# Optimization experiments

Measured on AMD Instinct MI355X. Metric: run time of the kernel, lower is better.

Reference implementation:

```python
import jax, jax.numpy as jnp
import numpy as np


def setup_inputs() -> dict:
    key = jax.random.key(0)
    k1, k2, k3 = jax.random.split(key, 3)
    d = 256
    x = jax.random.normal(k1, (8, 2048, d), dtype=jnp.float32)
    # torch nn.Linear(d, d, bias=False) weights, shape [out, in]
    Wq = jax.random.normal(k2, (d, d), dtype=jnp.float32) * (d ** -0.5)
    Wk = jax.random.normal(k3, (d, d), dtype=jnp.float32) * (d ** -0.5)
    return {"x": x, "Wq": Wq, "Wk": Wk}


def reference(x, Wq, Wk):
    # q = x @ Wq^T, k = x @ Wk^T (torch Linear convention), v = x (raw context)
    d = x.shape[-1]
    scale = d ** -0.5
    q = jnp.einsum('bnd,ed->bne', x, Wq)
    k = jnp.einsum('bnd,ed->bne', x, Wk)
    sim = jnp.einsum('bid,bjd->bij', q, k) * scale  # [b, n, n]
    attn = jax.nn.softmax(sim, axis=-1)
    out = jnp.einsum('bij,bjd->bid', attn, x)
    return out
```

## Files before the change

### kernel.cpp

```cpp
#include <hip/hip_runtime.h>
#include <hip/hip_bf16.h>

#define BB 8
#define NN 2048
#define DD 256

typedef _Float16 half8 __attribute__((ext_vector_type(8)));
typedef _Float16 half4 __attribute__((ext_vector_type(4)));
typedef float f32x4 __attribute__((ext_vector_type(4)));
typedef unsigned int uint4v __attribute__((ext_vector_type(4)));

#define GLDS(gsrc, ldst) __builtin_amdgcn_global_load_lds( \
    (const __attribute__((address_space(1))) void*)(gsrc), \
    (__attribute__((address_space(3))) void*)(ldst), 16, 0, 0)

__device__ __forceinline__ half8 cvt8(const float* __restrict__ p) {
    f32x4 a = *(const f32x4*)p;
    f32x4 b = *(const f32x4*)(p + 4);
    half8 h;
    h[0] = (_Float16)a[0]; h[1] = (_Float16)a[1];
    h[2] = (_Float16)a[2]; h[3] = (_Float16)a[3];
    h[4] = (_Float16)b[0]; h[5] = (_Float16)b[1];
    h[6] = (_Float16)b[2]; h[7] = (_Float16)b[3];
    return h;
}

__global__ void __launch_bounds__(256)
qk_proj(const float* __restrict__ x, const float* __restrict__ Wq,
        const float* __restrict__ Wk, _Float16* __restrict__ qh,
        _Float16* __restrict__ kh, _Float16* __restrict__ xT) {
    __shared__ __align__(16) _Float16 Wql[16][264];
    __shared__ __align__(16) _Float16 Wkl[16][264];
    const int tid = threadIdx.x;
    const int wave = tid >> 6, lane = tid & 63;
    const int g = lane >> 4, l16 = lane & 15;
    const int rowblk = blockIdx.x >> 1, thalf = blockIdx.x & 1;
    const size_t r0 = ((size_t)rowblk * 4 + wave) * 16;

    half8 xa[8];
#pragma unroll
    for (int c = 0; c < 8; ++c)
        xa[c] = cvt8(x + (r0 + l16) * DD + c * 32 + g * 8);

    {
        const int gt = (int)(r0 + l16);
        const int bb = gt >> 11, nn = gt & 2047;
        _Float16* xtb = xT + (size_t)bb * DD * NN + nn;
        if (thalf == 0) {
#pragma unroll
            for (int c = 0; c < 4; ++c)
#pragma unroll
                for (int j = 0; j < 8; ++j)
                    xtb[(size_t)(c * 32 + g * 8 + j) * NN] = xa[c][j];
        } else {
#pragma unroll
            for (int c = 4; c < 8; ++c)
#pragma unroll
                for (int j = 0; j < 8; ++j)
                    xtb[(size_t)(c * 32 + g * 8 + j) * NN] = xa[c][j];
        }
    }

    for (int i = 0; i < 8; ++i) {
        const int t = thalf * 8 + i;
        __syncthreads();
        {
            const int sel = tid >> 7;
            const int tt  = tid & 127;
            const int row = tt >> 3;
            const int col = (tt & 7) * 32;
            const float* src = (sel ? Wk : Wq) + (size_t)(t * 16 + row) * DD + col;
            _Float16* dst = sel ? &Wkl[row][col] : &Wql[row][col];
#pragma unroll
            for (int j = 0; j < 4; ++j)
                *(half8*)(dst + j * 8) = cvt8(src + j * 8);
        }
        __syncthreads();
        f32x4 aq = {0.f, 0.f, 0.f, 0.f}, ak = {0.f, 0.f, 0.f, 0.f};
#pragma unroll
        for (int c = 0; c < 8; ++c) {
            half8 bq = *(const half8*)&Wql[l16][c * 32 + g * 8];
            half8 bk = *(const half8*)&Wkl[l16][c * 32 + g * 8];
            aq = __builtin_amdgcn_mfma_f32_16x16x32_f16(xa[c], bq, aq, 0, 0, 0);
            ak = __builtin_amdgcn_mfma_f32_16x16x32_f16(xa[c], bk, ak, 0, 0, 0);
        }
#pragma unroll
        for (int r = 0; r < 4; ++r) {
            size_t row = r0 + g * 4 + r;
            qh[row * DD + t * 16 + l16] = (_Float16)(aq[r] * 0.0625f);
            kh[row * DD + t * 16 + l16] = (_Float16)ak[r];
        }
    }
}

__global__ void __launch_bounds__(512)
attn(const _Float16* __restrict__ qh, const _Float16* __restrict__ kh,
     const _Float16* __restrict__ xT, float* __restrict__ out,
     _Float16* __restrict__ Op, float* __restrict__ ml, int lgS) {
    __shared__ __align__(16) _Float16 Kl[2][32 * 256];
    __shared__ __align__(16) _Float16 Vl[3][256 * 32];
    const int tid = threadIdx.x;
    const int wave = tid >> 6, lane = tid & 63;
    const int g = lane >> 4, l16 = lane & 15;
    const int S = 1 << lgS;
    const int b = blockIdx.x & 7;
    const int tt = blockIdx.x >> 3;
    const int s = tt & (S - 1);
    const int qb = tt >> lgS;
    const int wq0 = qb * 256 + wave * 32;
    const int kvlen = NN >> lgS;
    const int kv_begin = s * kvlen;
    const int nt = kvlen >> 5;

    const _Float16* qp = qh + ((size_t)b * NN + wq0) * DD;
    const _Float16* kb = kh + (size_t)b * NN * DD;
    const _Float16* vb = xT + (size_t)b * DD * NN;

    int krow[2], koff[2], vrow[2];
#pragma unroll
    for (int j = 0; j < 2; ++j) {
        int rp = 8 * j + wave;
        int T = 2 * rp + (lane >> 5);
        krow[j] = 8 * ((T >> 2) & 3) + 4 * (T >> 4) + (T & 3);
        koff[j] = ((lane & 31) * 8) ^ ((T & 7) << 3);
        vrow[j] = 16 * rp + (lane >> 2);
    }
    const int voff = (lane & 3) * 8;

    half8 qf[2][8];
#pragma unroll
    for (int t = 0; t < 2; ++t)
#pragma unroll
        for (int c = 0; c < 8; ++c)
            qf[t][c] = *(const half8*)(qp + (size_t)(t * 16 + l16) * DD + c * 32 + g * 8);

    f32x4 O[2][16];
    f32x4 zero = {0.f, 0.f, 0.f, 0.f};
#pragma unroll
    for (int t = 0; t < 2; ++t)
#pragma unroll
        for (int dt = 0; dt < 16; ++dt) O[t][dt] = zero;
    float m[2] = {-1e30f, -1e30f};
    float l[2] = {0.f, 0.f};
    half8 paA[2], paB[2];

    f32x4 s00, s01, s10, s11;
    auto qkt = [&](int tau) {
        const _Float16* Klb = Kl[tau & 1];
        s00 = zero; s01 = zero; s10 = zero; s11 = zero;
        const int swz = (l16 & 7) << 3;
#pragma unroll
        for (int c = 0; c < 8; ++c) {
            int u = (c * 32 + g * 8) ^ swz;
            half8 k0 = *(const half8*)&Klb[l16 * 256 + u];
            half8 k1 = *(const half8*)&Klb[(16 + l16) * 256 + u];
            s00 = __builtin_amdgcn_mfma_f32_16x16x32_f16(k0, qf[0][c], s00, 0, 0, 0);
            s01 = __builtin_amdgcn_mfma_f32_16x16x32_f16(k1, qf[0][c], s01, 0, 0, 0);
            s10 = __builtin_amdgcn_mfma_f32_16x16x32_f16(k0, qf[1][c], s10, 0, 0, 0);
            s11 = __builtin_amdgcn_mfma_f32_16x16x32_f16(k1, qf[1][c], s11, 0, 0, 0);
        }
    };

    auto pv = [&](int tau, half8 (&paIn)[2]) {
        const _Float16* Vlb = Vl[tau % 3];
#pragma unroll
        for (int dt = 0; dt < 16; ++dt) {
            half8 vf = *(const half8*)&Vlb[(dt * 16 + l16) * 32 + g * 8];
            O[0][dt] = __builtin_amdgcn_mfma_f32_16x16x32_f16(paIn[0], vf, O[0][dt], 0, 0, 0);
            O[1][dt] = __builtin_amdgcn_mfma_f32_16x16x32_f16(paIn[1], vf, O[1][dt], 0, 0, 0);
        }
    };

    auto smax = [&](half8 (&paOut)[2]) {
        float tm[2];
#pragma unroll
        for (int t = 0; t < 2; ++t) {
            const f32x4& a = t ? s10 : s00;
            const f32x4& c = t ? s11 : s01;
            float v = fmaxf(fmaxf(fmaxf(a[0], a[1]), fmaxf(a[2], a[3])),
                            fmaxf(fmaxf(c[0], c[1]), fmaxf(c[2], c[3])));
            v = fmaxf(v, __shfl_xor(v, 16));
            v = fmaxf(v, __shfl_xor(v, 32));
            tm[t] = v;
        }
        bool need = (tm[0] > m[0] + 8.f) || (tm[1] > m[1] + 8.f);
        if (__ballot(need)) {
#pragma unroll
            for (int t = 0; t < 2; ++t) {
                float nm = fmaxf(m[t], tm[t]);
                float al = __expf(m[t] - nm);
                m[t] = nm;
                l[t] *= al;
                float alr[4];
#pragma unroll
                for (int r = 0; r < 4; ++r) alr[r] = __shfl(al, g * 4 + r);
#pragma unroll
                for (int dt = 0; dt < 16; ++dt)
#pragma unroll
                    for (int r = 0; r < 4; ++r) O[t][dt][r] *= alr[r];
            }
        }
#pragma unroll
        for (int t = 0; t < 2; ++t) {
            f32x4 e0, e1;
            const f32x4& a = t ? s10 : s00;
            const f32x4& c = t ? s11 : s01;
#pragma unroll
            for (int r = 0; r < 4; ++r) {
                e0[r] = __expf(a[r] - m[t]);
                e1[r] = __expf(c[r] - m[t]);
            }
            float rs = (e0[0] + e0[1]) + (e0[2] + e0[3]) +
                       (e1[0] + e1[1]) + (e1[2] + e1[3]);
            rs += __shfl_xor(rs, 16);
            rs += __shfl_xor(rs, 32);
            l[t] += rs;

            uint4v w;
            w[0] = __builtin_bit_cast(unsigned, __builtin_amdgcn_cvt_pkrtz(e0[0], e0[1]));
            w[1] = __builtin_bit_cast(unsigned, __builtin_amdgcn_cvt_pkrtz(e0[2], e0[3]));
            w[2] = __builtin_bit_cast(unsigned, __builtin_amdgcn_cvt_pkrtz(e1[0], e1[1]));
            w[3] = __builtin_bit_cast(unsigned, __builtin_amdgcn_cvt_pkrtz(e1[2], e1[3]));
            paOut[t] = __builtin_bit_cast(half8, w);
        }
    };

    auto issue = [&](int tau) {
        _Float16* kdst = Kl[tau & 1];
        _Float16* vdst = Vl[tau % 3];
        const int kvn = kv_begin + (tau << 5);
#pragma unroll
        for (int j = 0; j < 2; ++j) {
            int rp = 8 * j + wave;
            GLDS(kb + (size_t)(kvn + krow[j]) * DD + koff[j], kdst + rp * 512);
            GLDS(vb + (size_t)vrow[j] * NN + kvn + voff,      vdst + rp * 512);
        }
    };

    auto body = [&](int tau, half8 (&paIn)[2], half8 (&paOut)[2]) {
        __syncthreads();
        if (tau + 1 < nt) issue(tau + 1);
        qkt(tau);
        pv(tau - 1, paIn);
        smax(paOut);
    };

    issue(0);
    __syncthreads();
    issue(1);
    qkt(0);
    smax(paA);

    int tau = 1;
    for (; tau + 1 < nt - 1; tau += 2) {
        body(tau, paA, paB);
        body(tau + 1, paB, paA);
    }
    body(nt - 1, paA, paB);
    pv(nt - 1, paB);

    if (lgS == 0) {
#pragma unroll
        for (int t = 0; t < 2; ++t) {
            float rl = 1.0f / l[t];
            float rlr[4];
#pragma unroll
            for (int r = 0; r < 4; ++r) rlr[r] = __shfl(rl, g * 4 + r);
            float* ob = out + ((size_t)b * NN + wq0 + t * 16) * DD;
#pragma unroll
            for (int dt = 0; dt < 16; ++dt)
#pragma unroll
                for (int r = 0; r < 4; ++r)
                    ob[(size_t)(g * 4 + r) * DD + dt * 16 + l16] = O[t][dt][r] * rlr[r];
        }
    } else {
#pragma unroll
        for (int t = 0; t < 2; ++t) {
            float rl = 1.0f / l[t];
            float rlr[4];
#pragma unroll
            for (int r = 0; r < 4; ++r) rlr[r] = __shfl(rl, g * 4 + r);
            _Float16* ow = Op + (((size_t)s * BB + b) * NN + wq0 + t * 16) * DD;
#pragma unroll
            for (int dt = 0; dt < 16; ++dt)
#pragma unroll
                for (int r = 0; r < 4; ++r)
                    ow[(dt * 4 + r) * 64 + lane] = (_Float16)(O[t][dt][r] * rlr[r]);
        }
        if (lane < 16) {
            float* mlp = ml + (((size_t)s * BB + b) * NN + wq0) * 2;
#pragma unroll
            for (int t = 0; t < 2; ++t) {
                mlp[(t * 16 + lane) * 2]     = m[t];
                mlp[(t * 16 + lane) * 2 + 1] = l[t];
            }
        }
    }
}

__global__ void __launch_bounds__(256)
combine(const _Float16* __restrict__ Op, const float* __restrict__ ml,
        float* __restrict__ out, int S) {
    const int b = blockIdx.x & 7;
    const int k = blockIdx.x >> 3;
    const int row = b * NN + k * 4 + (threadIdx.x >> 6);
    const int c0  = (threadIdx.x & 63) * 4;
    const int widx = ((c0 >> 4) * 4 + (row & 3)) * 64 + ((row >> 2) & 3) * 16 + (c0 & 15);
    const size_t rbase = (size_t)(row & ~15) * DD + widx;

    float M = -1e30f;
    for (int s = 0; s < S; ++s)
        M = fmaxf(M, ml[((size_t)s * BB * NN + row) * 2]);
    float wsum = 0.f;
    f32x4 acc = {0.f, 0.f, 0.f, 0.f};
    for (int s = 0; s < S; ++s) {
        const float* mlp = ml + ((size_t)s * BB * NN + row) * 2;
        float w = __expf(mlp[0] - M) * mlp[1];
        wsum += w;
        half4 o = *(const half4*)(Op + (size_t)s * BB * NN * DD + rbase);
        acc[0] += w * (float)o[0]; acc[1] += w * (float)o[1];
        acc[2] += w * (float)o[2]; acc[3] += w * (float)o[3];
    }
    float inv = 1.0f / wsum;
    f32x4 res = {acc[0] * inv, acc[1] * inv, acc[2] * inv, acc[3] * inv};
    *(f32x4*)(out + (size_t)row * DD + c0) = res;
}

extern "C" void kernel_launch(void* const* d_in, const int* in_sizes, int n_in,
                              void* d_out, int out_size, void* d_ws, size_t ws_size,
                              hipStream_t stream) {
    const float* x  = (const float*)d_in[0];
    const float* Wq = (const float*)d_in[1];
    const float* Wk = (const float*)d_in[2];
    float* out = (float*)d_out;

    const size_t NTOK = (size_t)BB * NN;
    const size_t HBUF = NTOK * DD * sizeof(_Float16);
    _Float16* qh = (_Float16*)d_ws;
    _Float16* kh = qh + NTOK * DD;
    _Float16* xT = kh + NTOK * DD;
    const size_t base = 3 * HBUF;
    const size_t OSZ  = NTOK * DD * sizeof(_Float16);
    const size_t MLSZ = NTOK * 2 * sizeof(float);

    int lgS = 0;
    if (ws_size >= base + 4 * (OSZ + MLSZ)) lgS = 2;
    else if (ws_size >= base + 2 * (OSZ + MLSZ)) lgS = 1;
    const int S = 1 << lgS;

    _Float16* Op = (_Float16*)((char*)d_ws + base);
    float* ml = (float*)((char*)d_ws + base + (size_t)S * OSZ);

    qk_proj<<<dim3(BB * NN / 64 * 2), dim3(256), 0, stream>>>(x, Wq, Wk, qh, kh, xT);
    attn<<<dim3(BB * (NN / 256) * S), dim3(512), 0, stream>>>(qh, kh, xT, out, Op, ml, lgS);
    if (S > 1)
        combine<<<dim3(BB * NN / 4), dim3(256), 0, stream>>>(Op, ml, out, S);
}
```

Before: 91.63 us.

## Double-buffer weight tiles in projection and fold log2e into Q for exp2 softmax

```diff
diff --git a/kernel.cpp b/kernel.cpp
--- a/kernel.cpp
+++ b/kernel.cpp
@@ -29,13 +29,13 @@
 qk_proj(const float* __restrict__ x, const float* __restrict__ Wq,
         const float* __restrict__ Wk, _Float16* __restrict__ qh,
         _Float16* __restrict__ kh, _Float16* __restrict__ xT) {
-    __shared__ __align__(16) _Float16 Wql[16][264];
-    __shared__ __align__(16) _Float16 Wkl[16][264];
+    __shared__ __align__(16) _Float16 Wl[2][2][16][264];
     const int tid = threadIdx.x;
     const int wave = tid >> 6, lane = tid & 63;
     const int g = lane >> 4, l16 = lane & 15;
     const int rowblk = blockIdx.x >> 1, thalf = blockIdx.x & 1;
     const size_t r0 = ((size_t)rowblk * 4 + wave) * 16;
+    const float QSCALE = 0.0625f * 1.44269504f;
 
     half8 xa[8];
 #pragma unroll
@@ -61,35 +61,55 @@
         }
     }
 
+    const int sel = tid >> 7;
+    const int tt  = tid & 127;
+    const int wrow = tt >> 3;
+    const int wcol = (tt & 7) * 32;
+
+    f32x4 wreg[8];
+    auto issueLoads = [&](int t) {
+        const float* src = (sel ? Wk : Wq) + (size_t)(t * 16 + wrow) * DD + wcol;
+#pragma unroll
+        for (int j = 0; j < 8; ++j)
+            wreg[j] = *(const f32x4*)(src + j * 4);
+    };
+    auto writeLDS = [&](int buf) {
+        _Float16* dst = &Wl[buf][sel][wrow][wcol];
+#pragma unroll
+        for (int j = 0; j < 4; ++j) {
+            half8 h;
+#pragma unroll
+            for (int i2 = 0; i2 < 4; ++i2) {
+                h[i2]     = (_Float16)wreg[2 * j][i2];
+                h[4 + i2] = (_Float16)wreg[2 * j + 1][i2];
+            }
+            *(half8*)(dst + j * 8) = h;
+        }
+    };
+
+    issueLoads(thalf * 8);
+    writeLDS(0);
+    __syncthreads();
+
     for (int i = 0; i < 8; ++i) {
         const int t = thalf * 8 + i;
-        __syncthreads();
-        {
-            const int sel = tid >> 7;
-            const int tt  = tid & 127;
-            const int row = tt >> 3;
-            const int col = (tt & 7) * 32;
-            const float* src = (sel ? Wk : Wq) + (size_t)(t * 16 + row) * DD + col;
-            _Float16* dst = sel ? &Wkl[row][col] : &Wql[row][col];
-#pragma unroll
-            for (int j = 0; j < 4; ++j)
-                *(half8*)(dst + j * 8) = cvt8(src + j * 8);
-        }
-        __syncthreads();
+        if (i + 1 < 8) issueLoads(t + 1);
         f32x4 aq = {0.f, 0.f, 0.f, 0.f}, ak = {0.f, 0.f, 0.f, 0.f};
 #pragma unroll
         for (int c = 0; c < 8; ++c) {
-            half8 bq = *(const half8*)&Wql[l16][c * 32 + g * 8];
-            half8 bk = *(const half8*)&Wkl[l16][c * 32 + g * 8];
+            half8 bq = *(const half8*)&Wl[i & 1][0][l16][c * 32 + g * 8];
+            half8 bk = *(const half8*)&Wl[i & 1][1][l16][c * 32 + g * 8];
             aq = __builtin_amdgcn_mfma_f32_16x16x32_f16(xa[c], bq, aq, 0, 0, 0);
             ak = __builtin_amdgcn_mfma_f32_16x16x32_f16(xa[c], bk, ak, 0, 0, 0);
         }
 #pragma unroll
         for (int r = 0; r < 4; ++r) {
             size_t row = r0 + g * 4 + r;
-            qh[row * DD + t * 16 + l16] = (_Float16)(aq[r] * 0.0625f);
+            qh[row * DD + t * 16 + l16] = (_Float16)(aq[r] * QSCALE);
             kh[row * DD + t * 16 + l16] = (_Float16)ak[r];
         }
+        if (i + 1 < 8) writeLDS((i + 1) & 1);
+        __syncthreads();
     }
 }
 
@@ -188,7 +208,7 @@
 #pragma unroll
             for (int t = 0; t < 2; ++t) {
                 float nm = fmaxf(m[t], tm[t]);
-                float al = __expf(m[t] - nm);
+                float al = exp2f(m[t] - nm);
                 m[t] = nm;
                 l[t] *= al;
                 float alr[4];
@@ -207,8 +227,8 @@
             const f32x4& c = t ? s11 : s01;
 #pragma unroll
             for (int r = 0; r < 4; ++r) {
-                e0[r] = __expf(a[r] - m[t]);
-                e1[r] = __expf(c[r] - m[t]);
+                e0[r] = exp2f(a[r] - m[t]);
+                e1[r] = exp2f(c[r] - m[t]);
             }
             float rs = (e0[0] + e0[1]) + (e0[2] + e0[3]) +
                        (e1[0] + e1[1]) + (e1[2] + e1[3]);
@@ -315,7 +335,7 @@
     f32x4 acc = {0.f, 0.f, 0.f, 0.f};
     for (int s = 0; s < S; ++s) {
         const float* mlp = ml + ((size_t)s * BB * NN + row) * 2;
-        float w = __expf(mlp[0] - M) * mlp[1];
+        float w = exp2f(mlp[0] - M) * mlp[1];
         wsum += w;
         half4 o = *(const half4*)(Op + (size_t)s * BB * NN * DD + rbase);
         acc[0] += w * (float)o[0]; acc[1] += w * (float)o[1];
```

New measurement: 100.0 us. +9.2%, slower.
